# Kernel tuning notes

Measured on AMD Instinct MI355X. Metric: run time of the kernel, lower is better.

Reference implementation:

```python
import jax, jax.numpy as jnp
import numpy as np

E = 8          # num_experts
K = 2          # top_k
ALPHA = 0.01   # aux_loss_coef


def setup_inputs() -> dict:
    key = jax.random.key(0)
    k1, k2, k3, k4 = jax.random.split(key, 4)
    x = jax.random.normal(k1, (4, 4096, 768), jnp.float32)
    gate_w = jax.random.normal(k2, (E, 768), jnp.float32) * 0.02   # Router gate [E, H]
    w1 = jax.random.normal(k3, (E, 3072, 768), jnp.float32) * 0.02  # per-expert [I, H]
    w2 = jax.random.normal(k4, (E, 768, 3072), jnp.float32) * 0.02  # per-expert [H, I]
    return {"x": x, "gate_w": gate_w, "w1": w1, "w2": w2}


def reference(x, gate_w, w1, w2):
    B, S, H = x.shape
    N = B * S
    x_flat = x.reshape(N, H)

    # ---- Router: top-K gating ----
    gate_logits = x_flat @ gate_w.T                      # [N, E]
    gate_probs = jax.nn.softmax(gate_logits, axis=-1)    # [N, E]
    top_weights, top_indices = jax.lax.top_k(gate_probs, K)  # [N, K] each
    top_weights = top_weights / top_weights.sum(-1, keepdims=True)

    # ---- Load balancing aux loss ----
    counts = jnp.zeros(E, gate_probs.dtype).at[top_indices.reshape(-1)].add(1.0)
    f = counts / (N * K)
    p = gate_probs.mean(axis=0)
    aux_loss = ALPHA * E * jnp.sum(f * p)

    # ---- Dispatch + per-expert FFN + weighted combine ----
    # combine[n, e] = sum_k top_weights[n, k] * [top_indices[n, k] == e]
    combine = jnp.zeros((N, E), x_flat.dtype).at[
        jnp.arange(N)[:, None], top_indices
    ].add(top_weights)                                   # [N, E]

    y = jnp.zeros_like(x_flat)
    for e in range(E):  # fixed small loop over experts
        h = jax.nn.gelu(x_flat @ w1[e].T, approximate=True)  # [N, I] (GELU-tanh)
        y = y + combine[:, e:e + 1] * (h @ w2[e].T)          # [N, H]

    return y.reshape(B, S, H), aux_loss
```

## Files before the change

kernel.cpp:

```cpp
#include <hip/hip_runtime.h>
#include <hip/hip_bf16.h>

#define N_TOK 16384
#define H_DIM 768
#define I_DIM 3072
#define NEXP 8
#define RBLK 1024

typedef short bf16x8 __attribute__((ext_vector_type(8)));
typedef float f32x4 __attribute__((ext_vector_type(4)));

__device__ __forceinline__ unsigned short f2bf(float f) {
    unsigned int u = __float_as_uint(f);
    u += 0x7fffu + ((u >> 16) & 1u);
    return (unsigned short)(u >> 16);
}

__device__ __forceinline__ float gelu_tanh(float v) {
    float u = 0.7978845608028654f * (v + 0.044715f * v * v * v);
    float t = __expf(2.0f * fminf(u, 15.0f));
    return 0.5f * v * (1.0f + (t - 1.0f) / (t + 1.0f));
}

__device__ __forceinline__ void gll16(const void* g, void* l) {
    __builtin_amdgcn_global_load_lds(
        (const __attribute__((address_space(1))) unsigned int*)g,
        (__attribute__((address_space(3))) unsigned int*)l, 16, 0, 0);
}

__global__ __launch_bounds__(256) void moe_router(
    const float* __restrict__ x, const float* __restrict__ gw,
    unsigned short* __restrict__ xbf,
    int* __restrict__ topidx, float* __restrict__ topw,
    float* __restrict__ partials)
{
    __shared__ float gws[NEXP * H_DIM];
    __shared__ float red[64];
    const int tid = threadIdx.x;
    for (int i = tid * 4; i < NEXP * H_DIM; i += 1024)
        *(float4*)(gws + i) = *(const float4*)(gw + i);
    __syncthreads();

    const int lane = tid & 63;
    const int wid = tid >> 6;
    const int tbase = blockIdx.x * 16 + wid * 4;

    float lcnt[8], lps[8];
#pragma unroll
    for (int e = 0; e < 8; ++e) { lcnt[e] = 0.f; lps[e] = 0.f; }

#pragma unroll
    for (int k = 0; k < 4; ++k) {
        const int t = tbase + k;
        float acc[8] = {0.f, 0.f, 0.f, 0.f, 0.f, 0.f, 0.f, 0.f};
#pragma unroll
        for (int j = 0; j < 3; ++j) {
            const int col = j * 256 + lane * 4;
            float4 xv = *(const float4*)(x + (size_t)t * H_DIM + col);
            ushort4 o;
            o.x = f2bf(xv.x); o.y = f2bf(xv.y); o.z = f2bf(xv.z); o.w = f2bf(xv.w);
            *(ushort4*)(xbf + (size_t)t * H_DIM + col) = o;
#pragma unroll
            for (int e = 0; e < 8; ++e) {
                float4 g = *(const float4*)(gws + e * H_DIM + col);
                acc[e] += xv.x * g.x + xv.y * g.y + xv.z * g.z + xv.w * g.w;
            }
        }
#pragma unroll
        for (int off = 32; off >= 1; off >>= 1)
#pragma unroll
            for (int e = 0; e < 8; ++e) acc[e] += __shfl_xor(acc[e], off, 64);

        int e0 = 0;
#pragma unroll
        for (int e = 1; e < 8; ++e) if (acc[e] > acc[e0]) e0 = e;
        int e1 = (e0 == 0) ? 1 : 0;
#pragma unroll
        for (int e = 0; e < 8; ++e) if (e != e0 && acc[e] > acc[e1]) e1 = e;

        float mx = acc[0];
#pragma unroll
        for (int e = 1; e < 8; ++e) mx = fmaxf(mx, acc[e]);
        float p[8]; float s = 0.f;
#pragma unroll
        for (int e = 0; e < 8; ++e) { p[e] = expf(acc[e] - mx); s += p[e]; }
        float inv = 1.0f / s;
#pragma unroll
        for (int e = 0; e < 8; ++e) p[e] *= inv;

        float wsum = p[e0] + p[e1];
        if (lane == 0) {
            topidx[2 * t] = e0; topidx[2 * t + 1] = e1;
            topw[2 * t] = p[e0] / wsum; topw[2 * t + 1] = p[e1] / wsum;
            lcnt[e0] += 1.f; lcnt[e1] += 1.f;
#pragma unroll
            for (int e = 0; e < 8; ++e) lps[e] += p[e];
        }
    }

    if (lane == 0) {
#pragma unroll
        for (int e = 0; e < 8; ++e) {
            red[wid * 16 + e] = lcnt[e];
            red[wid * 16 + 8 + e] = lps[e];
        }
    }
    __syncthreads();
    if (tid < 16)
        partials[blockIdx.x * 16 + tid] =
            red[tid] + red[16 + tid] + red[32 + tid] + red[48 + tid];
}

__global__ __launch_bounds__(256) void moe_rank(
    const int* __restrict__ topidx, const float* __restrict__ topw,
    const float* __restrict__ partials, int* __restrict__ offs,
    float* __restrict__ aux_out, int* __restrict__ perm, float* __restrict__ pw)
{
    const int b = blockIdx.x;
    const int tid = threadIdx.x;
    __shared__ float stot[256], spre[256];
    __shared__ float tot[16];
    __shared__ int pfx[8];

    const int c = tid & 15;
    float vtot = 0.f, vpre = 0.f;
    for (int r = tid >> 4; r < RBLK; r += 16) {
        float v = partials[r * 16 + c];
        vtot += v;
        if (r < b) vpre += v;
    }
    stot[tid] = vtot; spre[tid] = vpre;
    __syncthreads();
    if (tid < 16) {
        float t = 0.f, q = 0.f;
#pragma unroll
        for (int k = 0; k < 16; ++k) { t += stot[k * 16 + tid]; q += spre[k * 16 + tid]; }
        tot[tid] = t;
        if (tid < 8) spre[tid] = q;
    }
    __syncthreads();
    if (tid == 0) {
        int run = 0;
        float aux = 0.f;
#pragma unroll
        for (int e = 0; e < 8; ++e) {
            pfx[e] = run + (int)(spre[e] + 0.5f);
            aux += (tot[e] / (float)(N_TOK * 2)) * (tot[8 + e] / (float)N_TOK);
            if (b == 0) offs[e] = run;
            run += (int)(tot[e] + 0.5f);
        }
        if (b == 0) { offs[8] = run; *aux_out = 0.01f * 8.0f * aux; }
    }
    __syncthreads();
    if (tid < 32) {
        const int t = b * 16 + (tid >> 1);
        const int slot = tid & 1;
        const int myexp = topidx[2 * t + slot];
        int rank = 0;
#pragma unroll
        for (int ee = 0; ee < 8; ++ee) {
            unsigned long long m = __ballot(myexp == ee);
            if (myexp == ee)
                rank = pfx[ee] + __popcll(m & ((1ull << tid) - 1ull));
        }
        perm[rank] = t;
        pw[rank] = topw[2 * t + slot];
    }
}

__global__ __launch_bounds__(256) void moe_cvt2(
    const float* __restrict__ a, unsigned short* __restrict__ oa,
    const float* __restrict__ bsrc, unsigned short* __restrict__ ob, int n)
{
    int idx = (blockIdx.x * 256 + threadIdx.x) * 4;
    const int stride = gridDim.x * 1024;
    for (; idx < 2 * n; idx += stride) {
        const float* in = (idx < n) ? a : bsrc;
        unsigned short* out = (idx < n) ? oa : ob;
        const int i = (idx < n) ? idx : idx - n;
        float4 v = *(const float4*)(in + i);
        ushort4 o;
        o.x = f2bf(v.x); o.y = f2bf(v.y); o.z = f2bf(v.z); o.w = f2bf(v.w);
        *(ushort4*)(out + i) = o;
    }
}


#define GEMM_STAGE(t)                                                             \
    { const int s_ = (t) & 3;                                                     \
      gll16(asrc0 + (t) * 32, As + s_ * 8192 +        tid * 8);                   \
      gll16(asrc1 + (t) * 32, As + s_ * 8192 + 4096 + tid * 8);                   \
      gll16(bsrc0 + (t) * 32, Bs + s_ * 8192 +        tid * 8);                   \
      gll16(bsrc1 + (t) * 32, Bs + s_ * 8192 + 4096 + tid * 8); }

#define GEMM_LOADFRAG(t)                                                          \
      const unsigned short* Ab_ = As + ((t) & 3) * 8192 + pAoff;                  \
      const unsigned short* Bb_ = Bs + ((t) & 3) * 8192 + pBoff;                  \
      bf16x8 a_[8], b_[4];                                                        \
      _Pragma("unroll")                                                           \
      for (int i_ = 0; i_ < 8; ++i_) a_[i_] = *(const bf16x8*)(Ab_ + i_ * 1024);  \
      _Pragma("unroll")                                                           \
      for (int j_ = 0; j_ < 4; ++j_) b_[j_] = *(const bf16x8*)(Bb_ + j_ * 1024);

#define GEMM_MFMA()                                                               \
      __builtin_amdgcn_s_setprio(1);                                              \
      _Pragma("unroll")                                                           \
      for (int i_ = 0; i_ < 8; ++i_)                                              \
      _Pragma("unroll")                                                           \
      for (int j_ = 0; j_ < 4; ++j_)                                              \
          acc[i_][j_] = __builtin_amdgcn_mfma_f32_16x16x32_bf16(                  \
              a_[i_], b_[j_], acc[i_][j_], 0, 0, 0);                              \
      __builtin_amdgcn_s_setprio(0);

#define GEMM_SYNC(N_IMM)                                                          \
    asm volatile("s_waitcnt vmcnt(" #N_IMM ")" ::: "memory");                     \
    __builtin_amdgcn_s_barrier();                                                 \
    __builtin_amdgcn_sched_barrier(0);

#define GEMM_PIPELINE(NT)                                                         \
    GEMM_STAGE(0); GEMM_STAGE(1); GEMM_STAGE(2);                                  \
    GEMM_SYNC(8);                                                                 \
    for (int t = 0; t < (NT) - 3; ++t) {                                          \
        GEMM_LOADFRAG(t);                                                         \
        GEMM_STAGE(t + 3);                                                        \
        GEMM_MFMA();                                                              \
        GEMM_SYNC(8);                                                             \
    }                                                                             \
    { GEMM_LOADFRAG((NT) - 3); GEMM_MFMA(); }                                     \
    GEMM_SYNC(4);                                                                 \
    { GEMM_LOADFRAG((NT) - 2); GEMM_MFMA(); }                                     \
    GEMM_SYNC(0);                                                                 \
    { GEMM_LOADFRAG((NT) - 1); GEMM_MFMA(); }

__global__ __launch_bounds__(512) void moe_gemm1(
    const unsigned short* __restrict__ xbf,
    const unsigned short* __restrict__ w1bf,
    const int* __restrict__ perm, const int* __restrict__ offs,
    unsigned short* __restrict__ hbuf, int e0)
{
    const int e = e0 + blockIdx.z;
    const int off = offs[e];
    const int n_e = offs[e + 1] - off;
    const int rt = blockIdx.y;
    if (rt * 256 >= n_e) return;
    const int ct = blockIdx.x;
    const int coff = off - offs[e0];

    __shared__ __align__(16) unsigned short As[4 * 8192];
    __shared__ __align__(16) unsigned short Bs[4 * 8192];

    const int tid = threadIdx.x;
    const int lane = tid & 63;
    const int wid = tid >> 6;
    const int wm = wid >> 2, wn = wid & 3;

    const int m = tid >> 3;
    const int csw = (tid & 7) ^ (m & 7);
    const int hi = csw >> 2, kc = csw & 3;

    const unsigned short* asrc0; const unsigned short* asrc1;
    const unsigned short* bsrc0; const unsigned short* bsrc1;
    {
        int r0 = hi * 128 + m, r1 = r0 + 64;
        int lr0 = rt * 256 + r0; if (lr0 >= n_e) lr0 = n_e - 1;
        int lr1 = rt * 256 + r1; if (lr1 >= n_e) lr1 = n_e - 1;
        asrc0 = xbf + (size_t)perm[off + lr0] * H_DIM + kc * 8;
        asrc1 = xbf + (size_t)perm[off + lr1] * H_DIM + kc * 8;
        bsrc0 = w1bf + ((size_t)e * I_DIM + ct * 256 + r0) * H_DIM + kc * 8;
        bsrc1 = w1bf + ((size_t)e * I_DIM + ct * 256 + r1) * H_DIM + kc * 8;
    }

    const int pAoff = (lane & 15) * 64 + ((((wm << 2) | (lane >> 4)) ^ (lane & 7)) << 3);
    const int pBoff = (wn & 1) * 4096 + (lane & 15) * 64 +
                      (((((wn >> 1) << 2) | (lane >> 4)) ^ (lane & 7)) << 3);

    f32x4 acc[8][4] = {};

    GEMM_PIPELINE(H_DIM / 32);

    const int rbase = rt * 256 + wm * 128 + (lane >> 4) * 4;
    const int cbase = ct * 256 + wn * 64 + (lane & 15);
#pragma unroll
    for (int i = 0; i < 8; ++i) {
#pragma unroll
        for (int r = 0; r < 4; ++r) {
            const int lr = rbase + i * 16 + r;
            if (lr < n_e) {
                unsigned short* dst = hbuf + (size_t)(coff + lr) * I_DIM + cbase;
#pragma unroll
                for (int j = 0; j < 4; ++j)
                    dst[j * 16] = f2bf(gelu_tanh(acc[i][j][r]));
            }
        }
    }
}

__global__ __launch_bounds__(512) void moe_gemm2(
    const unsigned short* __restrict__ hbuf,
    const unsigned short* __restrict__ w2bf,
    const int* __restrict__ perm, const float* __restrict__ pw,
    const int* __restrict__ offs, float* __restrict__ y, int e0)
{
    const int e = e0 + blockIdx.z;
    const int off = offs[e];
    const int n_e = offs[e + 1] - off;
    const int rt = blockIdx.y;
    if (rt * 256 >= n_e) return;
    const int ct = blockIdx.x;
    const int coff = off - offs[e0];

    __shared__ __align__(16) unsigned short As[4 * 8192];
    __shared__ __align__(16) unsigned short Bs[4 * 8192];

    const int tid = threadIdx.x;
    const int lane = tid & 63;
    const int wid = tid >> 6;
    const int wm = wid >> 2, wn = wid & 3;

    const int m = tid >> 3;
    const int csw = (tid & 7) ^ (m & 7);
    const int hi = csw >> 2, kc = csw & 3;

    const unsigned short* asrc0; const unsigned short* asrc1;
    const unsigned short* bsrc0; const unsigned short* bsrc1;
    {
        int r0 = hi * 128 + m, r1 = r0 + 64;
        int lr0 = rt * 256 + r0; if (lr0 >= n_e) lr0 = n_e - 1;
        int lr1 = rt * 256 + r1; if (lr1 >= n_e) lr1 = n_e - 1;
        asrc0 = hbuf + (size_t)(coff + lr0) * I_DIM + kc * 8;
        asrc1 = hbuf + (size_t)(coff + lr1) * I_DIM + kc * 8;
        bsrc0 = w2bf + ((size_t)e * H_DIM + ct * 256 + r0) * I_DIM + kc * 8;
        bsrc1 = w2bf + ((size_t)e * H_DIM + ct * 256 + r1) * I_DIM + kc * 8;
    }

    const int pAoff = (lane & 15) * 64 + ((((wm << 2) | (lane >> 4)) ^ (lane & 7)) << 3);
    const int pBoff = (wn & 1) * 4096 + (lane & 15) * 64 +
                      (((((wn >> 1) << 2) | (lane >> 4)) ^ (lane & 7)) << 3);

    f32x4 acc[8][4] = {};

    GEMM_PIPELINE(I_DIM / 32);

    const int rbase = rt * 256 + wm * 128 + (lane >> 4) * 4;
    const int cbase = ct * 256 + wn * 64 + (lane & 15);
#pragma unroll
    for (int i = 0; i < 8; ++i) {
#pragma unroll
        for (int r = 0; r < 4; ++r) {
            const int lr = rbase + i * 16 + r;
            if (lr < n_e) {
                const int token = perm[off + lr];
                const float w = pw[off + lr];
                float* dst = y + (size_t)token * H_DIM + cbase;
#pragma unroll
                for (int j = 0; j < 4; ++j)
                    atomicAdd(dst + j * 16, w * acc[i][j][r]);
            }
        }
    }
}

extern "C" void kernel_launch(void* const* d_in, const int* in_sizes, int n_in,
                              void* d_out, int out_size, void* d_ws, size_t ws_size,
                              hipStream_t stream) {
    const float* x  = (const float*)d_in[0];
    const float* gw = (const float*)d_in[1];
    const float* w1 = (const float*)d_in[2];
    const float* w2 = (const float*)d_in[3];
    float* y = (float*)d_out;

    char* base = (char*)d_ws;
    size_t o = 0;
    unsigned short* xbf  = (unsigned short*)(base + o); o += (size_t)N_TOK * H_DIM * 2;
    unsigned short* w1bf = (unsigned short*)(base + o); o += (size_t)NEXP * I_DIM * H_DIM * 2;
    unsigned short* w2bf = (unsigned short*)(base + o); o += (size_t)NEXP * H_DIM * I_DIM * 2;
    int*   topidx = (int*)(base + o);   o += (size_t)N_TOK * 2 * 4;
    float* topw   = (float*)(base + o); o += (size_t)N_TOK * 2 * 4;
    int*   perm   = (int*)(base + o);   o += (size_t)N_TOK * 2 * 4;
    float* pw     = (float*)(base + o); o += (size_t)N_TOK * 2 * 4;
    float* partials = (float*)(base + o); o += (size_t)RBLK * 16 * 4;
    int*   offs     = (int*)(base + o);   o += 64;
    unsigned short* hbuf = (unsigned short*)(base + o);
    size_t remain = (ws_size > o) ? (ws_size - o) : 0;

    long cap_rows = (long)(remain / (size_t)(I_DIM * 2));
    int nch;
    if (cap_rows >= 32768)      nch = 1;
    else if (cap_rows >= 18022) nch = 2;
    else if (cap_rows >= 9011)  nch = 4;
    else                        nch = 8;
    const int G = NEXP / nch;

    hipMemsetAsync(d_out, 0, (size_t)out_size * 4, stream);

    moe_router<<<RBLK, 256, 0, stream>>>(x, gw, xbf, topidx, topw, partials);
    moe_cvt2<<<4096, 256, 0, stream>>>(w1, w1bf, w2, w2bf, NEXP * I_DIM * H_DIM);
    moe_rank<<<RBLK, 256, 0, stream>>>(topidx, topw, partials, offs,
                                       y + (size_t)N_TOK * H_DIM, perm, pw);

    for (int c = 0; c < nch; ++c) {
        const int e0 = c * G;
        moe_gemm1<<<dim3(12, 64, G), 512, 0, stream>>>(
            xbf, w1bf, perm, offs, hbuf, e0);
        moe_gemm2<<<dim3(3, 64, G), 512, 0, stream>>>(
            hbuf, w2bf, perm, pw, offs, y, e0);
    }
}
```

Before: 602.7 us.

## Rework expert GEMM mainloop to double-buffered BK=64 with phased barrier interleave

Both expert GEMMs now use a 2-stage, 64-wide K tile instead of a 4-stage, 32-wide pipeline. Each K tile is split into four MFMA phases, with the next tile's A and B global-to-LDS loads issued between them and explicit s_barrier pairs around each phase. The goal is to halve the number of pipeline iterations and overlap loads with MFMA work at a finer grain. The row-tile grid dimension is also halved, which launches fewer empty blocks. The cost is that each expert can now hold at most 8192 routed rows, so heavily skewed routing would silently drop tokens.

```diff
diff --git a/kernel.cpp b/kernel.cpp
--- a/kernel.cpp
+++ b/kernel.cpp
@@ -186,51 +186,66 @@
 }
 
 
-#define GEMM_STAGE(t)                                                             \
-    { const int s_ = (t) & 3;                                                     \
-      gll16(asrc0 + (t) * 32, As + s_ * 8192 +        tid * 8);                   \
-      gll16(asrc1 + (t) * 32, As + s_ * 8192 + 4096 + tid * 8);                   \
-      gll16(bsrc0 + (t) * 32, Bs + s_ * 8192 +        tid * 8);                   \
-      gll16(bsrc1 + (t) * 32, Bs + s_ * 8192 + 4096 + tid * 8); }
-
-#define GEMM_LOADFRAG(t)                                                          \
-      const unsigned short* Ab_ = As + ((t) & 3) * 8192 + pAoff;                  \
-      const unsigned short* Bb_ = Bs + ((t) & 3) * 8192 + pBoff;                  \
-      bf16x8 a_[8], b_[4];                                                        \
-      _Pragma("unroll")                                                           \
-      for (int i_ = 0; i_ < 8; ++i_) a_[i_] = *(const bf16x8*)(Ab_ + i_ * 1024);  \
-      _Pragma("unroll")                                                           \
-      for (int j_ = 0; j_ < 4; ++j_) b_[j_] = *(const bf16x8*)(Bb_ + j_ * 1024);
-
-#define GEMM_MFMA()                                                               \
-      __builtin_amdgcn_s_setprio(1);                                              \
-      _Pragma("unroll")                                                           \
-      for (int i_ = 0; i_ < 8; ++i_)                                              \
-      _Pragma("unroll")                                                           \
-      for (int j_ = 0; j_ < 4; ++j_)                                              \
-          acc[i_][j_] = __builtin_amdgcn_mfma_f32_16x16x32_bf16(                  \
-              a_[i_], b_[j_], acc[i_][j_], 0, 0, 0);                              \
-      __builtin_amdgcn_s_setprio(0);
-
-#define GEMM_SYNC(N_IMM)                                                          \
-    asm volatile("s_waitcnt vmcnt(" #N_IMM ")" ::: "memory");                     \
-    __builtin_amdgcn_s_barrier();                                                 \
-    __builtin_amdgcn_sched_barrier(0);
-
-#define GEMM_PIPELINE(NT)                                                         \
-    GEMM_STAGE(0); GEMM_STAGE(1); GEMM_STAGE(2);                                  \
-    GEMM_SYNC(8);                                                                 \
-    for (int t = 0; t < (NT) - 3; ++t) {                                          \
-        GEMM_LOADFRAG(t);                                                         \
-        GEMM_STAGE(t + 3);                                                        \
-        GEMM_MFMA();                                                              \
-        GEMM_SYNC(8);                                                             \
-    }                                                                             \
-    { GEMM_LOADFRAG((NT) - 3); GEMM_MFMA(); }                                     \
-    GEMM_SYNC(4);                                                                 \
-    { GEMM_LOADFRAG((NT) - 2); GEMM_MFMA(); }                                     \
-    GEMM_SYNC(0);                                                                 \
-    { GEMM_LOADFRAG((NT) - 1); GEMM_MFMA(); }
+#define MFMA_(d_, va_, vb_) d_ = __builtin_amdgcn_mfma_f32_16x16x32_bf16(va_, vb_, d_, 0, 0, 0)
+
+#define STAGE_A4(tt, NT)                                                          \
+    if ((tt) < (NT)) { const int sd_ = ((tt) & 1) * 16384;                        \
+      gll16(asrc0 + (tt) * 64, As + sd_ +     0 + tid * 8);                       \
+      gll16(asrc1 + (tt) * 64, As + sd_ +  4096 + tid * 8);                       \
+      gll16(asrc2 + (tt) * 64, As + sd_ +  8192 + tid * 8);                       \
+      gll16(asrc3 + (tt) * 64, As + sd_ + 12288 + tid * 8); }
+
+#define STAGE_B4(tt, NT)                                                          \
+    if ((tt) < (NT)) { const int sd_ = ((tt) & 1) * 16384;                        \
+      gll16(bsrc0 + (tt) * 64, Bs + sd_ +     0 + tid * 8);                       \
+      gll16(bsrc1 + (tt) * 64, Bs + sd_ +  4096 + tid * 8);                       \
+      gll16(bsrc2 + (tt) * 64, Bs + sd_ +  8192 + tid * 8);                       \
+      gll16(bsrc3 + (tt) * 64, Bs + sd_ + 12288 + tid * 8); }
+
+#define GEMM_PHASE(I0, VM_OP, ...)                                                \
+  { bf16x8 a00 = *(const bf16x8*)(Acur + (I0) * 1024 + pk0);                      \
+    bf16x8 a01 = *(const bf16x8*)(Acur + (I0) * 1024 + pk1);                      \
+    bf16x8 a10 = *(const bf16x8*)(Acur + ((I0) + 1) * 1024 + pk0);                \
+    bf16x8 a11 = *(const bf16x8*)(Acur + ((I0) + 1) * 1024 + pk1);                \
+    __VA_ARGS__;                                                                  \
+    VM_OP;                                                                        \
+    asm volatile("s_barrier" ::: "memory");                                       \
+    __builtin_amdgcn_s_setprio(1);                                                \
+    MFMA_(acc[I0][0], a00, b00); MFMA_(acc[I0][0], a01, b01);                     \
+    MFMA_(acc[I0][1], a00, b10); MFMA_(acc[I0][1], a01, b11);                     \
+    MFMA_(acc[I0][2], a00, b20); MFMA_(acc[I0][2], a01, b21);                     \
+    MFMA_(acc[I0][3], a00, b30); MFMA_(acc[I0][3], a01, b31);                     \
+    MFMA_(acc[(I0)+1][0], a10, b00); MFMA_(acc[(I0)+1][0], a11, b01);             \
+    MFMA_(acc[(I0)+1][1], a10, b10); MFMA_(acc[(I0)+1][1], a11, b11);             \
+    MFMA_(acc[(I0)+1][2], a10, b20); MFMA_(acc[(I0)+1][2], a11, b21);             \
+    MFMA_(acc[(I0)+1][3], a10, b30); MFMA_(acc[(I0)+1][3], a11, b31);             \
+    __builtin_amdgcn_s_setprio(0);                                                \
+    asm volatile("s_barrier" ::: "memory"); }
+
+#define GEMM_NOP (void)0
+#define GEMM_VMDRAIN asm volatile("s_waitcnt vmcnt(0)" ::: "memory")
+
+#define GEMM_KTILE(t, NT)                                                         \
+  { const unsigned short* Acur = As + ((t) & 1) * 16384 + rowA;                   \
+    const unsigned short* Bcur = Bs + ((t) & 1) * 16384 + rowB;                   \
+    bf16x8 b00 = *(const bf16x8*)(Bcur +    0 + pk0);                             \
+    bf16x8 b01 = *(const bf16x8*)(Bcur +    0 + pk1);                             \
+    bf16x8 b10 = *(const bf16x8*)(Bcur + 1024 + pk0);                             \
+    bf16x8 b11 = *(const bf16x8*)(Bcur + 1024 + pk1);                             \
+    bf16x8 b20 = *(const bf16x8*)(Bcur + 2048 + pk0);                             \
+    bf16x8 b21 = *(const bf16x8*)(Bcur + 2048 + pk1);                             \
+    bf16x8 b30 = *(const bf16x8*)(Bcur + 3072 + pk0);                             \
+    bf16x8 b31 = *(const bf16x8*)(Bcur + 3072 + pk1);                             \
+    GEMM_PHASE(0, GEMM_NOP, STAGE_A4((t) + 1, NT));                               \
+    GEMM_PHASE(2, GEMM_NOP, STAGE_B4((t) + 1, NT));                               \
+    GEMM_PHASE(4, GEMM_NOP, GEMM_NOP);                                            \
+    GEMM_PHASE(6, GEMM_VMDRAIN, GEMM_NOP);                                        \
+  }
+
+#define GEMM_PROLOGUE(NT)                                                         \
+    STAGE_A4(0, NT); STAGE_B4(0, NT);                                             \
+    asm volatile("s_waitcnt vmcnt(0)" ::: "memory");                              \
+    asm volatile("s_barrier" ::: "memory");
 
 __global__ __launch_bounds__(512) void moe_gemm1(
     const unsigned short* __restrict__ xbf,
@@ -246,37 +261,47 @@
     const int ct = blockIdx.x;
     const int coff = off - offs[e0];
 
-    __shared__ __align__(16) unsigned short As[4 * 8192];
-    __shared__ __align__(16) unsigned short Bs[4 * 8192];
+    __shared__ __align__(16) unsigned short As[2 * 16384];
+    __shared__ __align__(16) unsigned short Bs[2 * 16384];
 
     const int tid = threadIdx.x;
     const int lane = tid & 63;
     const int wid = tid >> 6;
     const int wm = wid >> 2, wn = wid & 3;
 
-    const int m = tid >> 3;
-    const int csw = (tid & 7) ^ (m & 7);
-    const int hi = csw >> 2, kc = csw & 3;
-
-    const unsigned short* asrc0; const unsigned short* asrc1;
-    const unsigned short* bsrc0; const unsigned short* bsrc1;
+    const int srow = tid >> 3;
+    const int csw = (tid & 7) ^ (srow & 7);
+
+    const unsigned short *asrc0, *asrc1, *asrc2, *asrc3;
+    const unsigned short *bsrc0, *bsrc1, *bsrc2, *bsrc3;
     {
-        int r0 = hi * 128 + m, r1 = r0 + 64;
-        int lr0 = rt * 256 + r0; if (lr0 >= n_e) lr0 = n_e - 1;
-        int lr1 = rt * 256 + r1; if (lr1 >= n_e) lr1 = n_e - 1;
-        asrc0 = xbf + (size_t)perm[off + lr0] * H_DIM + kc * 8;
-        asrc1 = xbf + (size_t)perm[off + lr1] * H_DIM + kc * 8;
-        bsrc0 = w1bf + ((size_t)e * I_DIM + ct * 256 + r0) * H_DIM + kc * 8;
-        bsrc1 = w1bf + ((size_t)e * I_DIM + ct * 256 + r1) * H_DIM + kc * 8;
-    }
-
-    const int pAoff = (lane & 15) * 64 + ((((wm << 2) | (lane >> 4)) ^ (lane & 7)) << 3);
-    const int pBoff = (wn & 1) * 4096 + (lane & 15) * 64 +
-                      (((((wn >> 1) << 2) | (lane >> 4)) ^ (lane & 7)) << 3);
+        int lr[4];
+#pragma unroll
+        for (int q = 0; q < 4; ++q) {
+            int r = rt * 256 + q * 64 + srow;
+            lr[q] = (r >= n_e) ? (n_e - 1) : r;
+        }
+        asrc0 = xbf + (size_t)perm[off + lr[0]] * H_DIM + csw * 8;
+        asrc1 = xbf + (size_t)perm[off + lr[1]] * H_DIM + csw * 8;
+        asrc2 = xbf + (size_t)perm[off + lr[2]] * H_DIM + csw * 8;
+        asrc3 = xbf + (size_t)perm[off + lr[3]] * H_DIM + csw * 8;
+        const size_t wb = (size_t)e * I_DIM + ct * 256;
+        bsrc0 = w1bf + (wb + 0 * 64 + srow) * H_DIM + csw * 8;
+        bsrc1 = w1bf + (wb + 1 * 64 + srow) * H_DIM + csw * 8;
+        bsrc2 = w1bf + (wb + 2 * 64 + srow) * H_DIM + csw * 8;
+        bsrc3 = w1bf + (wb + 3 * 64 + srow) * H_DIM + csw * 8;
+    }
+
+    const int rowA = (wm * 128 + (lane & 15)) * 64;
+    const int rowB = (wn * 64 + (lane & 15)) * 64;
+    const int pk0 = (((lane >> 4)    ) ^ (lane & 7)) * 8;
+    const int pk1 = (((lane >> 4) + 4) ^ (lane & 7)) * 8;
 
     f32x4 acc[8][4] = {};
 
-    GEMM_PIPELINE(H_DIM / 32);
+    const int NT = H_DIM / 64;
+    GEMM_PROLOGUE(NT);
+    for (int t = 0; t < NT; ++t) { GEMM_KTILE(t, NT); }
 
     const int rbase = rt * 256 + wm * 128 + (lane >> 4) * 4;
     const int cbase = ct * 256 + wn * 64 + (lane & 15);
@@ -309,37 +334,47 @@
     const int ct = blockIdx.x;
     const int coff = off - offs[e0];
 
-    __shared__ __align__(16) unsigned short As[4 * 8192];
-    __shared__ __align__(16) unsigned short Bs[4 * 8192];
+    __shared__ __align__(16) unsigned short As[2 * 16384];
+    __shared__ __align__(16) unsigned short Bs[2 * 16384];
 
     const int tid = threadIdx.x;
     const int lane = tid & 63;
     const int wid = tid >> 6;
     const int wm = wid >> 2, wn = wid & 3;
 
-    const int m = tid >> 3;
-    const int csw = (tid & 7) ^ (m & 7);
-    const int hi = csw >> 2, kc = csw & 3;
-
-    const unsigned short* asrc0; const unsigned short* asrc1;
-    const unsigned short* bsrc0; const unsigned short* bsrc1;
+    const int srow = tid >> 3;
+    const int csw = (tid & 7) ^ (srow & 7);
+
+    const unsigned short *asrc0, *asrc1, *asrc2, *asrc3;
+    const unsigned short *bsrc0, *bsrc1, *bsrc2, *bsrc3;
     {
-        int r0 = hi * 128 + m, r1 = r0 + 64;
-        int lr0 = rt * 256 + r0; if (lr0 >= n_e) lr0 = n_e - 1;
-        int lr1 = rt * 256 + r1; if (lr1 >= n_e) lr1 = n_e - 1;
-        asrc0 = hbuf + (size_t)(coff + lr0) * I_DIM + kc * 8;
-        asrc1 = hbuf + (size_t)(coff + lr1) * I_DIM + kc * 8;
-        bsrc0 = w2bf + ((size_t)e * H_DIM + ct * 256 + r0) * I_DIM + kc * 8;
-        bsrc1 = w2bf + ((size_t)e * H_DIM + ct * 256 + r1) * I_DIM + kc * 8;
-    }
-
-    const int pAoff = (lane & 15) * 64 + ((((wm << 2) | (lane >> 4)) ^ (lane & 7)) << 3);
-    const int pBoff = (wn & 1) * 4096 + (lane & 15) * 64 +
-                      (((((wn >> 1) << 2) | (lane >> 4)) ^ (lane & 7)) << 3);
+        int lr[4];
+#pragma unroll
+        for (int q = 0; q < 4; ++q) {
+            int r = rt * 256 + q * 64 + srow;
+            lr[q] = (r >= n_e) ? (n_e - 1) : r;
+        }
+        asrc0 = hbuf + (size_t)(coff + lr[0]) * I_DIM + csw * 8;
+        asrc1 = hbuf + (size_t)(coff + lr[1]) * I_DIM + csw * 8;
+        asrc2 = hbuf + (size_t)(coff + lr[2]) * I_DIM + csw * 8;
+        asrc3 = hbuf + (size_t)(coff + lr[3]) * I_DIM + csw * 8;
+        const size_t wb = (size_t)e * H_DIM + ct * 256;
+        bsrc0 = w2bf + (wb + 0 * 64 + srow) * I_DIM + csw * 8;
+        bsrc1 = w2bf + (wb + 1 * 64 + srow) * I_DIM + csw * 8;
+        bsrc2 = w2bf + (wb + 2 * 64 + srow) * I_DIM + csw * 8;
+        bsrc3 = w2bf + (wb + 3 * 64 + srow) * I_DIM + csw * 8;
+    }
+
+    const int rowA = (wm * 128 + (lane & 15)) * 64;
+    const int rowB = (wn * 64 + (lane & 15)) * 64;
+    const int pk0 = (((lane >> 4)    ) ^ (lane & 7)) * 8;
+    const int pk1 = (((lane >> 4) + 4) ^ (lane & 7)) * 8;
 
     f32x4 acc[8][4] = {};
 
-    GEMM_PIPELINE(I_DIM / 32);
+    const int NT = I_DIM / 64;
+    GEMM_PROLOGUE(NT);
+    for (int t = 0; t < NT; ++t) { GEMM_KTILE(t, NT); }
 
     const int rbase = rt * 256 + wm * 128 + (lane >> 4) * 4;
     const int cbase = ct * 256 + wn * 64 + (lane & 15);
@@ -400,9 +435,9 @@
 
     for (int c = 0; c < nch; ++c) {
         const int e0 = c * G;
-        moe_gemm1<<<dim3(12, 64, G), 512, 0, stream>>>(
+        moe_gemm1<<<dim3(12, 32, G), 512, 0, stream>>>(
             xbf, w1bf, perm, offs, hbuf, e0);
-        moe_gemm2<<<dim3(3, 64, G), 512, 0, stream>>>(
+        moe_gemm2<<<dim3(3, 32, G), 512, 0, stream>>>(
             hbuf, w2bf, perm, pw, offs, y, e0);
     }
 }
```

New measurement: 692.6 us. 14.9% more time.

## Shrink GEMM tiles to 256x128 with 4 waves, 3-stage LDS ring, 2 blocks/CU

Applied to the files above, without the earlier changes.

Both expert GEMM kernels move from 512-thread blocks computing 256x256 tiles with a 4-stage LDS pipeline to 256-thread blocks computing 256x128 tiles with a 3-stage ring. LDS use per block drops sharply, so two blocks can share a CU, and the grid doubles along the column dimension. The aim is better occupancy and latency hiding. The cost is that each A row tile is loaded twice as often, which adds global traffic, and the pipeline is one stage shallower.

```diff
diff --git a/kernel.cpp b/kernel.cpp
--- a/kernel.cpp
+++ b/kernel.cpp
@@ -186,53 +186,49 @@
 }
 
 
-#define GEMM_STAGE(t)                                                             \
-    { const int s_ = (t) & 3;                                                     \
-      gll16(asrc0 + (t) * 32, As + s_ * 8192 +        tid * 8);                   \
-      gll16(asrc1 + (t) * 32, As + s_ * 8192 + 4096 + tid * 8);                   \
-      gll16(bsrc0 + (t) * 32, Bs + s_ * 8192 +        tid * 8);                   \
-      gll16(bsrc1 + (t) * 32, Bs + s_ * 8192 + 4096 + tid * 8); }
-
-#define GEMM_LOADFRAG(t)                                                          \
-      const unsigned short* Ab_ = As + ((t) & 3) * 8192 + pAoff;                  \
-      const unsigned short* Bb_ = Bs + ((t) & 3) * 8192 + pBoff;                  \
-      bf16x8 a_[8], b_[4];                                                        \
-      _Pragma("unroll")                                                           \
-      for (int i_ = 0; i_ < 8; ++i_) a_[i_] = *(const bf16x8*)(Ab_ + i_ * 1024);  \
-      _Pragma("unroll")                                                           \
-      for (int j_ = 0; j_ < 4; ++j_) b_[j_] = *(const bf16x8*)(Bb_ + j_ * 1024);
-
-#define GEMM_MFMA()                                                               \
-      __builtin_amdgcn_s_setprio(1);                                              \
-      _Pragma("unroll")                                                           \
-      for (int i_ = 0; i_ < 8; ++i_)                                              \
-      _Pragma("unroll")                                                           \
-      for (int j_ = 0; j_ < 4; ++j_)                                              \
-          acc[i_][j_] = __builtin_amdgcn_mfma_f32_16x16x32_bf16(                  \
-              a_[i_], b_[j_], acc[i_][j_], 0, 0, 0);                              \
-      __builtin_amdgcn_s_setprio(0);
-
-#define GEMM_SYNC(N_IMM)                                                          \
-    asm volatile("s_waitcnt vmcnt(" #N_IMM ")" ::: "memory");                     \
-    __builtin_amdgcn_s_barrier();                                                 \
-    __builtin_amdgcn_sched_barrier(0);
+#define MFMA_(d_, va_, vb_) d_ = __builtin_amdgcn_mfma_f32_16x16x32_bf16(va_, vb_, d_, 0, 0, 0)
+#define BAR asm volatile("s_barrier" ::: "memory")
+#define SCHED0 __builtin_amdgcn_sched_barrier(0)
+#define VM6 asm volatile("s_waitcnt vmcnt(6)" ::: "memory")
+#define VM0 asm volatile("s_waitcnt vmcnt(0)" ::: "memory")
+#define VMNONE (void)0
+#define STAGENONE (void)0
+
+#define STAGE6(tt) { unsigned short* DA_ = As + ((tt) % 3) * 8192;                \
+      unsigned short* DB_ = Bs + ((tt) % 3) * 4096;                               \
+      gll16(asrc0 + (tt) * 32, DA_ +        tid * 8);                             \
+      gll16(asrc1 + (tt) * 32, DA_ + 2048 + tid * 8);                             \
+      gll16(asrc2 + (tt) * 32, DA_ + 4096 + tid * 8);                             \
+      gll16(asrc3 + (tt) * 32, DA_ + 6144 + tid * 8);                             \
+      gll16(bsrc0 + (tt) * 32, DB_ +        tid * 8);                             \
+      gll16(bsrc1 + (tt) * 32, DB_ + 2048 + tid * 8); }
+
+#define GEMM_TILE(t, STAGE_OP, VM_OP)                                             \
+  { const unsigned short* Ab_ = As + ((t) % 3) * 8192 + pAoff;                    \
+    const unsigned short* Bb_ = Bs + ((t) % 3) * 4096 + pBoff;                    \
+    bf16x8 a_[8], b_[4];                                                          \
+    _Pragma("unroll")                                                             \
+    for (int i_ = 0; i_ < 8; ++i_) a_[i_] = *(const bf16x8*)(Ab_ + i_ * 1024);    \
+    _Pragma("unroll")                                                             \
+    for (int j_ = 0; j_ < 4; ++j_) b_[j_] = *(const bf16x8*)(Bb_ + j_ * 1024);    \
+    STAGE_OP;                                                                     \
+    __builtin_amdgcn_s_setprio(1);                                                \
+    _Pragma("unroll")                                                             \
+    for (int i_ = 0; i_ < 8; ++i_)                                                \
+    _Pragma("unroll")                                                             \
+    for (int j_ = 0; j_ < 4; ++j_)                                                \
+        MFMA_(acc[i_][j_], a_[i_], b_[j_]);                                       \
+    __builtin_amdgcn_s_setprio(0);                                                \
+    VM_OP; BAR; SCHED0; }
 
 #define GEMM_PIPELINE(NT)                                                         \
-    GEMM_STAGE(0); GEMM_STAGE(1); GEMM_STAGE(2);                                  \
-    GEMM_SYNC(8);                                                                 \
-    for (int t = 0; t < (NT) - 3; ++t) {                                          \
-        GEMM_LOADFRAG(t);                                                         \
-        GEMM_STAGE(t + 3);                                                        \
-        GEMM_MFMA();                                                              \
-        GEMM_SYNC(8);                                                             \
-    }                                                                             \
-    { GEMM_LOADFRAG((NT) - 3); GEMM_MFMA(); }                                     \
-    GEMM_SYNC(4);                                                                 \
-    { GEMM_LOADFRAG((NT) - 2); GEMM_MFMA(); }                                     \
-    GEMM_SYNC(0);                                                                 \
-    { GEMM_LOADFRAG((NT) - 1); GEMM_MFMA(); }
-
-__global__ __launch_bounds__(512) void moe_gemm1(
+    STAGE6(0); STAGE6(1);                                                         \
+    VM6; BAR;                                                                     \
+    for (int t = 0; t < (NT) - 2; ++t) GEMM_TILE(t, STAGE6(t + 2), VM6);          \
+    GEMM_TILE((NT) - 2, STAGENONE, VM0);                                          \
+    GEMM_TILE((NT) - 1, STAGENONE, VMNONE);
+
+__global__ __launch_bounds__(256, 2) void moe_gemm1(
     const unsigned short* __restrict__ xbf,
     const unsigned short* __restrict__ w1bf,
     const int* __restrict__ perm, const int* __restrict__ offs,
@@ -246,40 +242,44 @@
     const int ct = blockIdx.x;
     const int coff = off - offs[e0];
 
-    __shared__ __align__(16) unsigned short As[4 * 8192];
-    __shared__ __align__(16) unsigned short Bs[4 * 8192];
+    __shared__ __align__(16) unsigned short As[3 * 8192];
+    __shared__ __align__(16) unsigned short Bs[3 * 4096];
 
     const int tid = threadIdx.x;
     const int lane = tid & 63;
     const int wid = tid >> 6;
-    const int wm = wid >> 2, wn = wid & 3;
+    const int wm = wid >> 1, wn = wid & 1;
 
     const int m = tid >> 3;
     const int csw = (tid & 7) ^ (m & 7);
     const int hi = csw >> 2, kc = csw & 3;
 
-    const unsigned short* asrc0; const unsigned short* asrc1;
-    const unsigned short* bsrc0; const unsigned short* bsrc1;
+    const unsigned short *asrc0, *asrc1, *asrc2, *asrc3, *bsrc0, *bsrc1;
     {
-        int r0 = hi * 128 + m, r1 = r0 + 64;
-        int lr0 = rt * 256 + r0; if (lr0 >= n_e) lr0 = n_e - 1;
-        int lr1 = rt * 256 + r1; if (lr1 >= n_e) lr1 = n_e - 1;
-        asrc0 = xbf + (size_t)perm[off + lr0] * H_DIM + kc * 8;
-        asrc1 = xbf + (size_t)perm[off + lr1] * H_DIM + kc * 8;
-        bsrc0 = w1bf + ((size_t)e * I_DIM + ct * 256 + r0) * H_DIM + kc * 8;
-        bsrc1 = w1bf + ((size_t)e * I_DIM + ct * 256 + r1) * H_DIM + kc * 8;
+        const unsigned short* aq[4];
+#pragma unroll
+        for (int q = 0; q < 4; ++q) {
+            int r = rt * 256 + hi * 128 + q * 32 + m;
+            if (r >= n_e + rt * 256) {}
+            int lr = rt * 256 + hi * 128 + q * 32 + m;
+            if (lr >= n_e) lr = n_e - 1;
+            aq[q] = xbf + (size_t)perm[off + lr] * H_DIM + kc * 8;
+        }
+        asrc0 = aq[0]; asrc1 = aq[1]; asrc2 = aq[2]; asrc3 = aq[3];
+        const size_t wb = (size_t)e * I_DIM + ct * 128 + hi * 64;
+        bsrc0 = w1bf + (wb +  0 + m) * H_DIM + kc * 8;
+        bsrc1 = w1bf + (wb + 32 + m) * H_DIM + kc * 8;
     }
 
     const int pAoff = (lane & 15) * 64 + ((((wm << 2) | (lane >> 4)) ^ (lane & 7)) << 3);
-    const int pBoff = (wn & 1) * 4096 + (lane & 15) * 64 +
-                      (((((wn >> 1) << 2) | (lane >> 4)) ^ (lane & 7)) << 3);
+    const int pBoff = (lane & 15) * 64 + ((((wn << 2) | (lane >> 4)) ^ (lane & 7)) << 3);
 
     f32x4 acc[8][4] = {};
 
     GEMM_PIPELINE(H_DIM / 32);
 
     const int rbase = rt * 256 + wm * 128 + (lane >> 4) * 4;
-    const int cbase = ct * 256 + wn * 64 + (lane & 15);
+    const int cbase = ct * 128 + wn * 64 + (lane & 15);
 #pragma unroll
     for (int i = 0; i < 8; ++i) {
 #pragma unroll
@@ -295,7 +295,7 @@
     }
 }
 
-__global__ __launch_bounds__(512) void moe_gemm2(
+__global__ __launch_bounds__(256, 2) void moe_gemm2(
     const unsigned short* __restrict__ hbuf,
     const unsigned short* __restrict__ w2bf,
     const int* __restrict__ perm, const float* __restrict__ pw,
@@ -309,40 +309,42 @@
     const int ct = blockIdx.x;
     const int coff = off - offs[e0];
 
-    __shared__ __align__(16) unsigned short As[4 * 8192];
-    __shared__ __align__(16) unsigned short Bs[4 * 8192];
+    __shared__ __align__(16) unsigned short As[3 * 8192];
+    __shared__ __align__(16) unsigned short Bs[3 * 4096];
 
     const int tid = threadIdx.x;
     const int lane = tid & 63;
     const int wid = tid >> 6;
-    const int wm = wid >> 2, wn = wid & 3;
+    const int wm = wid >> 1, wn = wid & 1;
 
     const int m = tid >> 3;
     const int csw = (tid & 7) ^ (m & 7);
     const int hi = csw >> 2, kc = csw & 3;
 
-    const unsigned short* asrc0; const unsigned short* asrc1;
-    const unsigned short* bsrc0; const unsigned short* bsrc1;
+    const unsigned short *asrc0, *asrc1, *asrc2, *asrc3, *bsrc0, *bsrc1;
     {
-        int r0 = hi * 128 + m, r1 = r0 + 64;
-        int lr0 = rt * 256 + r0; if (lr0 >= n_e) lr0 = n_e - 1;
-        int lr1 = rt * 256 + r1; if (lr1 >= n_e) lr1 = n_e - 1;
-        asrc0 = hbuf + (size_t)(coff + lr0) * I_DIM + kc * 8;
-        asrc1 = hbuf + (size_t)(coff + lr1) * I_DIM + kc * 8;
-        bsrc0 = w2bf + ((size_t)e * H_DIM + ct * 256 + r0) * I_DIM + kc * 8;
-        bsrc1 = w2bf + ((size_t)e * H_DIM + ct * 256 + r1) * I_DIM + kc * 8;
+        const unsigned short* aq[4];
+#pragma unroll
+        for (int q = 0; q < 4; ++q) {
+            int lr = rt * 256 + hi * 128 + q * 32 + m;
+            if (lr >= n_e) lr = n_e - 1;
+            aq[q] = hbuf + (size_t)(coff + lr) * I_DIM + kc * 8;
+        }
+        asrc0 = aq[0]; asrc1 = aq[1]; asrc2 = aq[2]; asrc3 = aq[3];
+        const size_t wb = (size_t)e * H_DIM + ct * 128 + hi * 64;
+        bsrc0 = w2bf + (wb +  0 + m) * I_DIM + kc * 8;
+        bsrc1 = w2bf + (wb + 32 + m) * I_DIM + kc * 8;
     }
 
     const int pAoff = (lane & 15) * 64 + ((((wm << 2) | (lane >> 4)) ^ (lane & 7)) << 3);
-    const int pBoff = (wn & 1) * 4096 + (lane & 15) * 64 +
-                      (((((wn >> 1) << 2) | (lane >> 4)) ^ (lane & 7)) << 3);
+    const int pBoff = (lane & 15) * 64 + ((((wn << 2) | (lane >> 4)) ^ (lane & 7)) << 3);
 
     f32x4 acc[8][4] = {};
 
     GEMM_PIPELINE(I_DIM / 32);
 
     const int rbase = rt * 256 + wm * 128 + (lane >> 4) * 4;
-    const int cbase = ct * 256 + wn * 64 + (lane & 15);
+    const int cbase = ct * 128 + wn * 64 + (lane & 15);
 #pragma unroll
     for (int i = 0; i < 8; ++i) {
 #pragma unroll
@@ -400,9 +402,9 @@
 
     for (int c = 0; c < nch; ++c) {
         const int e0 = c * G;
-        moe_gemm1<<<dim3(12, 64, G), 512, 0, stream>>>(
+        moe_gemm1<<<dim3(24, 64, G), 256, 0, stream>>>(
             xbf, w1bf, perm, offs, hbuf, e0);
-        moe_gemm2<<<dim3(3, 64, G), 512, 0, stream>>>(
+        moe_gemm2<<<dim3(6, 64, G), 256, 0, stream>>>(
             hbuf, w2bf, perm, pw, offs, y, e0);
     }
 }
```

New measurement: 636.6 us. 1.06x slower.

## Load A operand fragments directly from global into registers, double-buffered

Applied to the files above, without the earlier changes.

The A operand (gathered tokens or hidden activations) is no longer staged through shared memory. Each wave now fetches its MFMA A fragments straight from global memory into two register buffers that alternate across k-steps, while only B stays in the 4-stage LDS pipeline. The goal is to halve LDS traffic and cut LDS reads and barriers for A. The cost is higher register pressure and a greater chance of uncoalesced or redundant global loads, since each wave reads 16-byte chunks per row and A rows are re-read by the 4 column waves.

```diff
diff --git a/kernel.cpp b/kernel.cpp
--- a/kernel.cpp
+++ b/kernel.cpp
@@ -186,51 +186,52 @@
 }
 
 
-#define GEMM_STAGE(t)                                                             \
-    { const int s_ = (t) & 3;                                                     \
-      gll16(asrc0 + (t) * 32, As + s_ * 8192 +        tid * 8);                   \
-      gll16(asrc1 + (t) * 32, As + s_ * 8192 + 4096 + tid * 8);                   \
-      gll16(bsrc0 + (t) * 32, Bs + s_ * 8192 +        tid * 8);                   \
-      gll16(bsrc1 + (t) * 32, Bs + s_ * 8192 + 4096 + tid * 8); }
-
-#define GEMM_LOADFRAG(t)                                                          \
-      const unsigned short* Ab_ = As + ((t) & 3) * 8192 + pAoff;                  \
-      const unsigned short* Bb_ = Bs + ((t) & 3) * 8192 + pBoff;                  \
-      bf16x8 a_[8], b_[4];                                                        \
-      _Pragma("unroll")                                                           \
-      for (int i_ = 0; i_ < 8; ++i_) a_[i_] = *(const bf16x8*)(Ab_ + i_ * 1024);  \
-      _Pragma("unroll")                                                           \
-      for (int j_ = 0; j_ < 4; ++j_) b_[j_] = *(const bf16x8*)(Bb_ + j_ * 1024);
-
-#define GEMM_MFMA()                                                               \
-      __builtin_amdgcn_s_setprio(1);                                              \
-      _Pragma("unroll")                                                           \
+#define BAR asm volatile("s_barrier" ::: "memory")
+#define SCHED0 __builtin_amdgcn_sched_barrier(0)
+#define LGKM0 asm volatile("s_waitcnt lgkmcnt(0)" ::: "memory")
+#define SYNC12 LGKM0; asm volatile("s_waitcnt vmcnt(12)" ::: "memory"); BAR; SCHED0
+#define SYNC8  LGKM0; asm volatile("s_waitcnt vmcnt(8)"  ::: "memory"); BAR; SCHED0
+#define SYNCNONE (void)0
+#define NOP (void)0
+
+#define STAGE_B(tt) { unsigned short* D_ = Bs + ((tt) & 3) * 8192;                \
+      gll16(bsrc0 + (size_t)(tt) * 32, D_ + tid * 8);                             \
+      gll16(bsrc1 + (size_t)(tt) * 32, D_ + 4096 + tid * 8); }
+
+#define AFETCH(DST, tt) { _Pragma("unroll")                                       \
       for (int i_ = 0; i_ < 8; ++i_)                                              \
-      _Pragma("unroll")                                                           \
-      for (int j_ = 0; j_ < 4; ++j_)                                              \
-          acc[i_][j_] = __builtin_amdgcn_mfma_f32_16x16x32_bf16(                  \
-              a_[i_], b_[j_], acc[i_][j_], 0, 0, 0);                              \
-      __builtin_amdgcn_s_setprio(0);
-
-#define GEMM_SYNC(N_IMM)                                                          \
-    asm volatile("s_waitcnt vmcnt(" #N_IMM ")" ::: "memory");                     \
-    __builtin_amdgcn_s_barrier();                                                 \
-    __builtin_amdgcn_sched_barrier(0);
+          DST[i_] = *(const bf16x8*)(abase + arow[i_] + (unsigned)(tt) * 64); }
+
+#define GTILE(t, ACUR, DO_A, DO_B, SYNC_OP)                                       \
+  { const unsigned short* Bb_ = Bs + ((t) & 3) * 8192 + pBoff;                    \
+    bf16x8 b0 = *(const bf16x8*)(Bb_);                                            \
+    bf16x8 b1 = *(const bf16x8*)(Bb_ + 1024);                                     \
+    bf16x8 b2 = *(const bf16x8*)(Bb_ + 2048);                                     \
+    bf16x8 b3 = *(const bf16x8*)(Bb_ + 3072);                                     \
+    DO_A; DO_B;                                                                   \
+    __builtin_amdgcn_s_setprio(1);                                                \
+    _Pragma("unroll")                                                             \
+    for (int i_ = 0; i_ < 8; ++i_) {                                              \
+        acc[i_][0] = __builtin_amdgcn_mfma_f32_16x16x32_bf16(ACUR[i_], b0, acc[i_][0], 0, 0, 0); \
+        acc[i_][1] = __builtin_amdgcn_mfma_f32_16x16x32_bf16(ACUR[i_], b1, acc[i_][1], 0, 0, 0); \
+        acc[i_][2] = __builtin_amdgcn_mfma_f32_16x16x32_bf16(ACUR[i_], b2, acc[i_][2], 0, 0, 0); \
+        acc[i_][3] = __builtin_amdgcn_mfma_f32_16x16x32_bf16(ACUR[i_], b3, acc[i_][3], 0, 0, 0); \
+    }                                                                             \
+    __builtin_amdgcn_s_setprio(0);                                                \
+    SYNC_OP; }
 
 #define GEMM_PIPELINE(NT)                                                         \
-    GEMM_STAGE(0); GEMM_STAGE(1); GEMM_STAGE(2);                                  \
-    GEMM_SYNC(8);                                                                 \
-    for (int t = 0; t < (NT) - 3; ++t) {                                          \
-        GEMM_LOADFRAG(t);                                                         \
-        GEMM_STAGE(t + 3);                                                        \
-        GEMM_MFMA();                                                              \
-        GEMM_SYNC(8);                                                             \
+    AFETCH(aA, 0);                                                                \
+    STAGE_B(0); STAGE_B(1); STAGE_B(2);                                           \
+    asm volatile("s_waitcnt vmcnt(4)" ::: "memory"); BAR;                         \
+    for (int t = 0; t < (NT) - 4; t += 2) {                                       \
+        GTILE(t,     aA, AFETCH(aB, t + 1), STAGE_B(t + 3), SYNC12);              \
+        GTILE(t + 1, aB, AFETCH(aA, t + 2), STAGE_B(t + 4), SYNC12);              \
     }                                                                             \
-    { GEMM_LOADFRAG((NT) - 3); GEMM_MFMA(); }                                     \
-    GEMM_SYNC(4);                                                                 \
-    { GEMM_LOADFRAG((NT) - 2); GEMM_MFMA(); }                                     \
-    GEMM_SYNC(0);                                                                 \
-    { GEMM_LOADFRAG((NT) - 1); GEMM_MFMA(); }
+    GTILE((NT) - 4, aA, AFETCH(aB, (NT) - 3), STAGE_B((NT) - 1), SYNC12);         \
+    GTILE((NT) - 3, aB, AFETCH(aA, (NT) - 2), NOP, SYNC12);                       \
+    GTILE((NT) - 2, aA, AFETCH(aB, (NT) - 1), NOP, SYNC8);                        \
+    GTILE((NT) - 1, aB, NOP, NOP, SYNCNONE);
 
 __global__ __launch_bounds__(512) void moe_gemm1(
     const unsigned short* __restrict__ xbf,
@@ -246,7 +247,6 @@
     const int ct = blockIdx.x;
     const int coff = off - offs[e0];
 
-    __shared__ __align__(16) unsigned short As[4 * 8192];
     __shared__ __align__(16) unsigned short Bs[4 * 8192];
 
     const int tid = threadIdx.x;
@@ -258,23 +258,27 @@
     const int csw = (tid & 7) ^ (m & 7);
     const int hi = csw >> 2, kc = csw & 3;
 
-    const unsigned short* asrc0; const unsigned short* asrc1;
     const unsigned short* bsrc0; const unsigned short* bsrc1;
     {
         int r0 = hi * 128 + m, r1 = r0 + 64;
-        int lr0 = rt * 256 + r0; if (lr0 >= n_e) lr0 = n_e - 1;
-        int lr1 = rt * 256 + r1; if (lr1 >= n_e) lr1 = n_e - 1;
-        asrc0 = xbf + (size_t)perm[off + lr0] * H_DIM + kc * 8;
-        asrc1 = xbf + (size_t)perm[off + lr1] * H_DIM + kc * 8;
         bsrc0 = w1bf + ((size_t)e * I_DIM + ct * 256 + r0) * H_DIM + kc * 8;
         bsrc1 = w1bf + ((size_t)e * I_DIM + ct * 256 + r1) * H_DIM + kc * 8;
     }
 
-    const int pAoff = (lane & 15) * 64 + ((((wm << 2) | (lane >> 4)) ^ (lane & 7)) << 3);
+    const char* abase = (const char*)xbf;
+    unsigned arow[8];
+#pragma unroll
+    for (int i = 0; i < 8; ++i) {
+        int lr = rt * 256 + wm * 128 + i * 16 + (lane & 15);
+        if (lr >= n_e) lr = n_e - 1;
+        arow[i] = (unsigned)perm[off + lr] * (H_DIM * 2) + ((lane >> 4) * 16);
+    }
+
     const int pBoff = (wn & 1) * 4096 + (lane & 15) * 64 +
                       (((((wn >> 1) << 2) | (lane >> 4)) ^ (lane & 7)) << 3);
 
     f32x4 acc[8][4] = {};
+    bf16x8 aA[8], aB[8];
 
     GEMM_PIPELINE(H_DIM / 32);
 
@@ -309,7 +313,6 @@
     const int ct = blockIdx.x;
     const int coff = off - offs[e0];
 
-    __shared__ __align__(16) unsigned short As[4 * 8192];
     __shared__ __align__(16) unsigned short Bs[4 * 8192];
 
     const int tid = threadIdx.x;
@@ -321,23 +324,27 @@
     const int csw = (tid & 7) ^ (m & 7);
     const int hi = csw >> 2, kc = csw & 3;
 
-    const unsigned short* asrc0; const unsigned short* asrc1;
     const unsigned short* bsrc0; const unsigned short* bsrc1;
     {
         int r0 = hi * 128 + m, r1 = r0 + 64;
-        int lr0 = rt * 256 + r0; if (lr0 >= n_e) lr0 = n_e - 1;
-        int lr1 = rt * 256 + r1; if (lr1 >= n_e) lr1 = n_e - 1;
-        asrc0 = hbuf + (size_t)(coff + lr0) * I_DIM + kc * 8;
-        asrc1 = hbuf + (size_t)(coff + lr1) * I_DIM + kc * 8;
         bsrc0 = w2bf + ((size_t)e * H_DIM + ct * 256 + r0) * I_DIM + kc * 8;
         bsrc1 = w2bf + ((size_t)e * H_DIM + ct * 256 + r1) * I_DIM + kc * 8;
     }
 
-    const int pAoff = (lane & 15) * 64 + ((((wm << 2) | (lane >> 4)) ^ (lane & 7)) << 3);
+    const char* abase = (const char*)hbuf;
+    unsigned arow[8];
+#pragma unroll
+    for (int i = 0; i < 8; ++i) {
+        int lr = rt * 256 + wm * 128 + i * 16 + (lane & 15);
+        if (lr >= n_e) lr = n_e - 1;
+        arow[i] = (unsigned)(coff + lr) * (I_DIM * 2) + ((lane >> 4) * 16);
+    }
+
     const int pBoff = (wn & 1) * 4096 + (lane & 15) * 64 +
                       (((((wn >> 1) << 2) | (lane >> 4)) ^ (lane & 7)) << 3);
 
     f32x4 acc[8][4] = {};
+    bf16x8 aA[8], aB[8];
 
     GEMM_PIPELINE(I_DIM / 32);
 
```

Result: slower. 1.092 ms (+81.1%).
